# Kernel tuning notes

Measured on AMD Instinct MI355X. Metric: run time of the kernel, lower is better.

## Reference

```python
import jax, jax.numpy as jnp
import numpy as np

N, DIN, DH, W = 256, 256, 512, 8

def _conv(x, w):
    # x: [N,C,H,W], w: [O,I,3,3], VALID conv (input already reflection-padded)
    return jax.lax.conv_general_dilated(x, w, (1, 1), 'VALID',
                                        dimension_numbers=('NCHW', 'OIHW', 'NCHW'))

def setup_inputs() -> dict:
    key = jax.random.key(0)
    ks = jax.random.split(key, 16)
    def cw(k, o, i):
        return jax.random.normal(k, (o, i, 3, 3), jnp.float32) * 0.02
    def cb(k, o):
        return jax.random.normal(k, (o,), jnp.float32) * 0.02
    return {
        'input': jax.random.normal(ks[0], (N, DIN, W, W), jnp.float32),
        'hidden_state': jax.random.normal(ks[1], (N, 2, DH, W, W), jnp.float32),
        'w_ii': cw(ks[2], DH, DIN), 'w_if': cw(ks[3], DH, DIN),
        'w_ig': cw(ks[4], DH, DIN), 'w_io': cw(ks[5], DH, DIN),
        'w_hi': cw(ks[6], DH, DH), 'w_hf': cw(ks[7], DH, DH),
        'w_hg': cw(ks[8], DH, DH), 'w_ho': cw(ks[9], DH, DH),
        'b_i': cb(ks[10], DH), 'b_f': cb(ks[11], DH),
        'b_g': cb(ks[12], DH), 'b_o': cb(ks[13], DH),
        'Wc_i': jax.random.normal(ks[14], (1, DH, W, W), jnp.float32) * 0.02,
        'Wc_f': jax.random.normal(ks[15], (1, DH, W, W), jnp.float32) * 0.02,
        'Wc_o': jax.random.normal(jax.random.fold_in(key, 99), (1, DH, W, W), jnp.float32) * 0.02,
    }

def reference(input, hidden_state, w_ii, w_if, w_ig, w_io, w_hi, w_hf, w_hg, w_ho,
              b_i, b_f, b_g, b_o, Wc_i, Wc_f, Wc_o):
    h0 = hidden_state[:, 0]
    c0 = hidden_state[:, 1]
    pad = ((0, 0), (0, 0), (1, 1), (1, 1))
    xp = jnp.pad(input, pad, mode='reflect')
    hp = jnp.pad(h0, pad, mode='reflect')
    # Fuse the 4 input convs and 4 hidden convs into two conv calls (linearity => same math).
    w_x = jnp.concatenate([w_ii, w_if, w_ig, w_io], axis=0)   # [4*DH, DIN, 3, 3]
    w_h = jnp.concatenate([w_hi, w_hf, w_hg, w_ho], axis=0)   # [4*DH, DH, 3, 3]
    b = jnp.concatenate([b_i, b_f, b_g, b_o], axis=0)         # [4*DH]
    pre = _conv(xp, w_x) + _conv(hp, w_h) + b[None, :, None, None]  # [N, 4*DH, 8, 8]
    pi, pf, pg, po = jnp.split(pre, 4, axis=1)
    i = jax.nn.sigmoid(pi + c0 * Wc_i)
    f = jax.nn.sigmoid(pf + c0 * Wc_f)
    g = jnp.tanh(pg)
    c_t = f * c0 + i * g
    o = jax.nn.sigmoid(po + c_t * Wc_o)
    h_t = o * jnp.tanh(c_t)
    hidden_state_out = jnp.stack([h_t, c_t], axis=1)  # [N, 2, DH, 8, 8]
    return (o, hidden_state_out)
```

## Files before the change

kernel.cpp:

```cpp
#include <hip/hip_runtime.h>
#include <hip/hip_bf16.h>


#define DEVINL __device__ __forceinline__

typedef __attribute__((ext_vector_type(8))) short short8;
typedef __attribute__((ext_vector_type(4))) float f32x4;
typedef __attribute__((ext_vector_type(4))) float float4v;

DEVINL unsigned short f2bf(float f) {
  union { float f; unsigned u; } x; x.f = f;
  unsigned r = x.u + 0x7fffu + ((x.u >> 16) & 1u);
  return (unsigned short)(r >> 16);
}

DEVINL void async16(const void* g, void* l) {
  __builtin_amdgcn_global_load_lds((const __attribute__((address_space(1))) void*)g,
                                   (__attribute__((address_space(3))) void*)l,
                                   16, 0, 0);
}

__global__ void __launch_bounds__(256) pack_p(const float* __restrict__ input,
                                              const float* __restrict__ hs,
                                              unsigned short* __restrict__ P) {
  int idx = blockIdx.x * 256 + threadIdx.x;
  int c = idx % 768;
  int n = idx / 768;
  const float* src;
  if (c < 256) src = input + (size_t)(n * 256 + c) * 64;
  else         src = hs + (size_t)n * 65536 + (size_t)(c - 256) * 64;

  float v[64];
#pragma unroll
  for (int i = 0; i < 16; ++i) {
    float4v q = *(const float4v*)(src + i * 4);
    v[i * 4 + 0] = q.x; v[i * 4 + 1] = q.y; v[i * 4 + 2] = q.z; v[i * 4 + 3] = q.w;
  }
  unsigned short bv[64];
#pragma unroll
  for (int i = 0; i < 64; ++i) bv[i] = f2bf(v[i]);

  size_t base = (size_t)n * 76800 + c;
#pragma unroll
  for (int yp = 0; yp < 10; ++yp) {
    const int ys = (yp == 0) ? 1 : ((yp == 9) ? 6 : yp - 1);
#pragma unroll
    for (int xp = 0; xp < 10; ++xp) {
      const int xs = (xp == 0) ? 1 : ((xp == 9) ? 6 : xp - 1);
      P[base + (yp * 10 + xp) * 768] = bv[ys * 8 + xs];
    }
  }
}

__global__ void __launch_bounds__(256) pack_w(const float* __restrict__ wx0, const float* __restrict__ wx1,
                                              const float* __restrict__ wx2, const float* __restrict__ wx3,
                                              const float* __restrict__ wh0, const float* __restrict__ wh1,
                                              const float* __restrict__ wh2, const float* __restrict__ wh3,
                                              unsigned short* __restrict__ Wb) {
  int idx = blockIdx.x * 256 + threadIdx.x;
  int c = idx % 768;
  int co = idx / 768;
  int gate = co >> 9, och = co & 511;
  const float* w;
  size_t wbase;
  if (c < 256) {
    w = (gate == 0) ? wx0 : (gate == 1) ? wx1 : (gate == 2) ? wx2 : wx3;
    wbase = (size_t)(och * 256 + c) * 9;
  } else {
    w = (gate == 0) ? wh0 : (gate == 1) ? wh1 : (gate == 2) ? wh2 : wh3;
    wbase = (size_t)(och * 512 + (c - 256)) * 9;
  }
  float v[9];
#pragma unroll
  for (int s = 0; s < 9; ++s) v[s] = w[wbase + s];
  size_t ob = (size_t)co * 6912 + c;
#pragma unroll
  for (int ky = 0; ky < 3; ++ky)
#pragma unroll
    for (int kx = 0; kx < 3; ++kx)
      Wb[ob + ky * 2304 + kx * 768] = f2bf(v[ky * 3 + kx]);
}

#define NT 108

__global__ void __launch_bounds__(512, 2) gemm_pre(const unsigned short* __restrict__ P,
                                                   const unsigned short* __restrict__ W,
                                                   float* __restrict__ pre) {
  __shared__ __align__(16) unsigned short lds[65536];

  const int t = threadIdx.x;
  const int l = t & 63;
  const int wid = t >> 6;
  const int wr = wid >> 2, wc = wid & 3;
  const int lm = l & 15, lk = l >> 4;

  int bid = blockIdx.x;
  const int x8 = bid & 7, j = bid >> 3;
  const int mb = x8 * 8 + (j & 7);
  const int nb = j >> 3;

  const int strow = t >> 2;
  const int stk = (((t & 3) ^ ((t >> 3) & 3)) << 3);
  const int am0 = mb * 256 + strow;
  const int am1 = am0 + 128;
  const int awin0 = ((am0 >> 6) * 100 + ((am0 >> 3) & 7) * 10 + (am0 & 7)) * 768 + stk;
  const int awin1 = ((am1 >> 6) * 100 + ((am1 >> 3) & 7) * 10 + (am1 & 7)) * 768 + stk;
  const size_t bb0 = (size_t)(nb * 256 + strow) * 6912 + stk;
  const size_t bb1 = bb0 + (size_t)128 * 6912;
  const int dstT = t * 8;

  const int swz = ((lk ^ ((lm >> 1) & 3)) << 3);
  const int aoffb = (wr * 128 + lm) * 32 + swz;
  const int boffb = 32768 + (wc * 64 + lm) * 32 + swz;

#define STAGE_A(TS, KS, D) { \
    int kg = (TS) * 64 + (KS) * 32; \
    int ky = kg / 2304; \
    int off = kg + ky * 5376; \
    async16(P + awin0 + off, &lds[(D) * 16384 + (KS) * 8192 + dstT]); \
    async16(P + awin1 + off, &lds[(D) * 16384 + (KS) * 8192 + 4096 + dstT]); }

#define STAGE_B(TS, KS, D) { \
    int kg = (TS) * 64 + (KS) * 32; \
    async16(W + bb0 + kg, &lds[32768 + (D) * 16384 + (KS) * 8192 + dstT]); \
    async16(W + bb1 + kg, &lds[32768 + (D) * 16384 + (KS) * 8192 + 4096 + dstT]); }

#define DS_A(D, KS, M) (*(const short8*)&lds[(D) * 16384 + (KS) * 8192 + (M) * 512 + aoffb])
#define DS_B(D, KS, Nn) (*(const short8*)&lds[(D) * 16384 + (KS) * 8192 + (Nn) * 512 + boffb])

#define LGKM0 asm volatile("s_waitcnt lgkmcnt(0)" ::: "memory")
#define VMC8  asm volatile("s_waitcnt vmcnt(8)" ::: "memory")

  f32x4 acc[8][4];
#pragma unroll
  for (int i = 0; i < 8; ++i)
#pragma unroll
    for (int n2 = 0; n2 < 4; ++n2) acc[i][n2] = (f32x4){0.f, 0.f, 0.f, 0.f};

  short8 a[4], b[4];

  STAGE_A(0, 0, 0); STAGE_B(0, 0, 0);
  STAGE_A(0, 1, 0); STAGE_B(0, 1, 0);
  STAGE_A(1, 0, 1); STAGE_B(1, 0, 1);
  VMC8;
  __builtin_amdgcn_s_barrier();

#define MFMA_BLK(MB) \
  _Pragma("unroll") for (int mm = 0; mm < 4; ++mm) \
  _Pragma("unroll") for (int nn = 0; nn < 4; ++nn) \
    acc[(MB) + mm][nn] = __builtin_amdgcn_mfma_f32_16x16x32_bf16(a[mm], b[nn], acc[(MB) + mm][nn], 0, 0, 0);

#pragma unroll 2
  for (int tau = 0; tau < NT; ++tau) {
    const int d = tau & 1;
    int t1 = tau + 1; if (t1 >= NT) t1 -= NT;
    int t2 = tau + 2; if (t2 >= NT) t2 -= NT;

#pragma unroll
    for (int mm = 0; mm < 4; ++mm) a[mm] = DS_A(d, 0, mm);
#pragma unroll
    for (int nn = 0; nn < 4; ++nn) b[nn] = DS_B(d, 0, nn);
    STAGE_A(t1, 1, d ^ 1);
    __builtin_amdgcn_s_barrier();
    LGKM0;
    __builtin_amdgcn_s_setprio(1);
    MFMA_BLK(0);
    __builtin_amdgcn_s_setprio(0);
    __builtin_amdgcn_s_barrier();

#pragma unroll
    for (int mm = 0; mm < 4; ++mm) a[mm] = DS_A(d, 0, 4 + mm);
    STAGE_B(t1, 1, d ^ 1);
    __builtin_amdgcn_s_barrier();
    LGKM0;
    __builtin_amdgcn_s_setprio(1);
    MFMA_BLK(4);
    __builtin_amdgcn_s_setprio(0);
    VMC8;
    __builtin_amdgcn_s_barrier();

#pragma unroll
    for (int mm = 0; mm < 4; ++mm) a[mm] = DS_A(d, 1, mm);
#pragma unroll
    for (int nn = 0; nn < 4; ++nn) b[nn] = DS_B(d, 1, nn);
    STAGE_A(t2, 0, d);
    __builtin_amdgcn_s_barrier();
    LGKM0;
    __builtin_amdgcn_s_setprio(1);
    MFMA_BLK(0);
    __builtin_amdgcn_s_setprio(0);
    __builtin_amdgcn_s_barrier();

#pragma unroll
    for (int mm = 0; mm < 4; ++mm) a[mm] = DS_A(d, 1, 4 + mm);
    STAGE_B(t2, 0, d);
    __builtin_amdgcn_s_barrier();
    LGKM0;
    __builtin_amdgcn_s_setprio(1);
    MFMA_BLK(4);
    __builtin_amdgcn_s_setprio(0);
    VMC8;
    __builtin_amdgcn_s_barrier();
  }

  const int r0 = mb * 256 + wr * 128 + lk * 4;
  const int cb = nb * 256 + wc * 64 + lm;
#pragma unroll
  for (int mm = 0; mm < 8; ++mm)
#pragma unroll
    for (int nn = 0; nn < 4; ++nn)
#pragma unroll
      for (int r = 0; r < 4; ++r)
        pre[(size_t)(r0 + mm * 16 + r) * 2048 + cb + nn * 16] = acc[mm][nn][r];
}

__global__ void __launch_bounds__(256) lstm_pointwise(const float* __restrict__ pre,
                                                      const float* __restrict__ hs,
                                                      const float* __restrict__ bi, const float* __restrict__ bf_,
                                                      const float* __restrict__ bg, const float* __restrict__ bo,
                                                      const float* __restrict__ wci, const float* __restrict__ wcf,
                                                      const float* __restrict__ wco,
                                                      float* __restrict__ out) {
  __shared__ float g[4][64][65];
  const int blk = blockIdx.x;
  const int n = blk >> 3, chb = blk & 7;
  const int t = threadIdx.x;

  {
    const int chl = t & 63, pr = t >> 6;
#pragma unroll
    for (int it = 0; it < 16; ++it) {
      int p = it * 4 + pr;
      size_t rowb = (size_t)(n * 64 + p) * 2048 + chb * 64 + chl;
      g[0][p][chl] = pre[rowb];
      g[1][p][chl] = pre[rowb + 512];
      g[2][p][chl] = pre[rowb + 1024];
      g[3][p][chl] = pre[rowb + 1536];
    }
  }
  __syncthreads();
  {
    const int pl = t & 63, chr = t >> 6;
#pragma unroll 4
    for (int it = 0; it < 16; ++it) {
      int chi = it * 4 + chr;
      int ch = chb * 64 + chi;
      int sp = ch * 64 + pl;
      float c0 = hs[(size_t)n * 65536 + 32768 + sp];
      float pi = g[0][pl][chi] + bi[ch];
      float pf = g[1][pl][chi] + bf_[ch];
      float pg = g[2][pl][chi] + bg[ch];
      float po = g[3][pl][chi] + bo[ch];
      float ig = 1.f / (1.f + __expf(-(pi + c0 * wci[sp])));
      float fg = 1.f / (1.f + __expf(-(pf + c0 * wcf[sp])));
      float gg = tanhf(pg);
      float ct = fg * c0 + ig * gg;
      float og = 1.f / (1.f + __expf(-(po + ct * wco[sp])));
      float ht = og * tanhf(ct);
      out[(size_t)(n * 512 + ch) * 64 + pl] = og;
      float* hso = out + 8388608;
      hso[(size_t)(n * 1024 + ch) * 64 + pl] = ht;
      hso[(size_t)(n * 1024 + 512 + ch) * 64 + pl] = ct;
    }
  }
}

extern "C" void kernel_launch(void* const* d_in, const int* in_sizes, int n_in,
                              void* d_out, int out_size, void* d_ws, size_t ws_size,
                              hipStream_t stream) {
  const float* input = (const float*)d_in[0];
  const float* hs    = (const float*)d_in[1];
  const float* wx0 = (const float*)d_in[2];
  const float* wx1 = (const float*)d_in[3];
  const float* wx2 = (const float*)d_in[4];
  const float* wx3 = (const float*)d_in[5];
  const float* wh0 = (const float*)d_in[6];
  const float* wh1 = (const float*)d_in[7];
  const float* wh2 = (const float*)d_in[8];
  const float* wh3 = (const float*)d_in[9];
  const float* bi  = (const float*)d_in[10];
  const float* bf_ = (const float*)d_in[11];
  const float* bg  = (const float*)d_in[12];
  const float* bo  = (const float*)d_in[13];
  const float* wci = (const float*)d_in[14];
  const float* wcf = (const float*)d_in[15];
  const float* wco = (const float*)d_in[16];
  float* out = (float*)d_out;

  float*          pre = (float*)d_ws;
  unsigned short* P   = (unsigned short*)((char*)d_ws + 134217728u);
  unsigned short* Wb  = (unsigned short*)((char*)d_ws + 134217728u + 39321600u);

  pack_p<<<768, 256, 0, stream>>>(input, hs, P);
  pack_w<<<6144, 256, 0, stream>>>(wx0, wx1, wx2, wx3, wh0, wh1, wh2, wh3, Wb);
  gemm_pre<<<512, 512, 0, stream>>>(P, Wb, pre);
  lstm_pointwise<<<2048, 256, 0, stream>>>(pre, hs, bi, bf_, bg, bo, wci, wcf, wco, out);
}
```

Baseline: 655.5 us.

## Fuse LSTM pointwise epilogue into GEMM by interleaving gate columns in weights

Reorders packed weight rows so that each 64-column group holds the i,f,g,o gates of 16 channels, which puts all four gates for one channel in the same wave's accumulators. The pointwise LSTM math then runs directly in the GEMM epilogue. This removes the 128MB fp32 pre-activation round trip and the separate pointwise kernel launch. It also swaps tanhf for an exp-based tanh, and the epilogue stores and c0/peephole loads are less coalesced than before.

```diff
diff --git a/kernel.cpp b/kernel.cpp
--- a/kernel.cpp
+++ b/kernel.cpp
@@ -13,6 +13,9 @@
   unsigned r = x.u + 0x7fffu + ((x.u >> 16) & 1u);
   return (unsigned short)(r >> 16);
 }
+
+DEVINL float sigm(float x) { return 1.f / (1.f + __expf(-x)); }
+DEVINL float tanh_fast(float x) { return 1.f - 2.f / (1.f + __expf(2.f * x)); }
 
 DEVINL void async16(const void* g, void* l) {
   __builtin_amdgcn_global_load_lds((const __attribute__((address_space(1))) void*)g,
@@ -73,7 +76,8 @@
   float v[9];
 #pragma unroll
   for (int s = 0; s < 9; ++s) v[s] = w[wbase + s];
-  size_t ob = (size_t)co * 6912 + c;
+  const int crow = (och >> 4) * 64 + gate * 16 + (och & 15);
+  size_t ob = (size_t)crow * 6912 + c;
 #pragma unroll
   for (int ky = 0; ky < 3; ++ky)
 #pragma unroll
@@ -83,9 +87,14 @@
 
 #define NT 108
 
-__global__ void __launch_bounds__(512, 2) gemm_pre(const unsigned short* __restrict__ P,
-                                                   const unsigned short* __restrict__ W,
-                                                   float* __restrict__ pre) {
+__global__ void __launch_bounds__(512, 2) gemm_lstm(const unsigned short* __restrict__ P,
+                                                    const unsigned short* __restrict__ W,
+                                                    const float* __restrict__ hs,
+                                                    const float* __restrict__ b_i, const float* __restrict__ b_f,
+                                                    const float* __restrict__ b_g, const float* __restrict__ b_o,
+                                                    const float* __restrict__ wci, const float* __restrict__ wcf,
+                                                    const float* __restrict__ wco,
+                                                    float* __restrict__ out) {
   __shared__ __align__(16) unsigned short lds[65536];
 
   const int t = threadIdx.x;
@@ -203,64 +212,31 @@
     __builtin_amdgcn_s_barrier();
   }
 
-  const int r0 = mb * 256 + wr * 128 + lk * 4;
-  const int cb = nb * 256 + wc * 64 + lm;
-#pragma unroll
-  for (int mm = 0; mm < 8; ++mm)
-#pragma unroll
-    for (int nn = 0; nn < 4; ++nn)
-#pragma unroll
-      for (int r = 0; r < 4; ++r)
-        pre[(size_t)(r0 + mm * 16 + r) * 2048 + cb + nn * 16] = acc[mm][nn][r];
-}
-
-__global__ void __launch_bounds__(256) lstm_pointwise(const float* __restrict__ pre,
-                                                      const float* __restrict__ hs,
-                                                      const float* __restrict__ bi, const float* __restrict__ bf_,
-                                                      const float* __restrict__ bg, const float* __restrict__ bo,
-                                                      const float* __restrict__ wci, const float* __restrict__ wcf,
-                                                      const float* __restrict__ wco,
-                                                      float* __restrict__ out) {
-  __shared__ float g[4][64][65];
-  const int blk = blockIdx.x;
-  const int n = blk >> 3, chb = blk & 7;
-  const int t = threadIdx.x;
-
-  {
-    const int chl = t & 63, pr = t >> 6;
-#pragma unroll
-    for (int it = 0; it < 16; ++it) {
-      int p = it * 4 + pr;
-      size_t rowb = (size_t)(n * 64 + p) * 2048 + chb * 64 + chl;
-      g[0][p][chl] = pre[rowb];
-      g[1][p][chl] = pre[rowb + 512];
-      g[2][p][chl] = pre[rowb + 1024];
-      g[3][p][chl] = pre[rowb + 1536];
-    }
-  }
-  __syncthreads();
-  {
-    const int pl = t & 63, chr = t >> 6;
-#pragma unroll 4
-    for (int it = 0; it < 16; ++it) {
-      int chi = it * 4 + chr;
-      int ch = chb * 64 + chi;
-      int sp = ch * 64 + pl;
-      float c0 = hs[(size_t)n * 65536 + 32768 + sp];
-      float pi = g[0][pl][chi] + bi[ch];
-      float pf = g[1][pl][chi] + bf_[ch];
-      float pg = g[2][pl][chi] + bg[ch];
-      float po = g[3][pl][chi] + bo[ch];
-      float ig = 1.f / (1.f + __expf(-(pi + c0 * wci[sp])));
-      float fg = 1.f / (1.f + __expf(-(pf + c0 * wcf[sp])));
-      float gg = tanhf(pg);
-      float ct = fg * c0 + ig * gg;
-      float og = 1.f / (1.f + __expf(-(po + ct * wco[sp])));
-      float ht = og * tanhf(ct);
-      out[(size_t)(n * 512 + ch) * 64 + pl] = og;
-      float* hso = out + 8388608;
-      hso[(size_t)(n * 1024 + ch) * 64 + pl] = ht;
-      hso[(size_t)(n * 1024 + 512 + ch) * 64 + pl] = ct;
+  const int ch = (nb * 4 + wc) * 16 + lm;
+  const int chp = ch * 64;
+  const float bI = b_i[ch], bF = b_f[ch], bG = b_g[ch], bO = b_o[ch];
+  float* hso = out + 8388608;
+#pragma unroll
+  for (int mm = 0; mm < 8; ++mm) {
+    const int n = mb * 4 + wr * 2 + (mm >> 2);
+    const float* c0p = hs + (size_t)n * 65536 + 32768 + chp;
+#pragma unroll
+    for (int r = 0; r < 4; ++r) {
+      const int p = (mm & 3) * 16 + lk * 4 + r;
+      const float c0 = c0p[p];
+      const float pi = acc[mm][0][r] + bI;
+      const float pf = acc[mm][1][r] + bF;
+      const float pg = acc[mm][2][r] + bG;
+      const float po = acc[mm][3][r] + bO;
+      const float ig = sigm(pi + c0 * wci[chp + p]);
+      const float fg = sigm(pf + c0 * wcf[chp + p]);
+      const float gg = tanh_fast(pg);
+      const float ct = fg * c0 + ig * gg;
+      const float og = sigm(po + ct * wco[chp + p]);
+      const float ht = og * tanh_fast(ct);
+      out[(size_t)n * 32768 + chp + p] = og;
+      hso[(size_t)n * 65536 + chp + p] = ht;
+      hso[(size_t)n * 65536 + 32768 + chp + p] = ct;
     }
   }
 }
@@ -287,12 +263,10 @@
   const float* wco = (const float*)d_in[16];
   float* out = (float*)d_out;
 
-  float*          pre = (float*)d_ws;
-  unsigned short* P   = (unsigned short*)((char*)d_ws + 134217728u);
-  unsigned short* Wb  = (unsigned short*)((char*)d_ws + 134217728u + 39321600u);
+  unsigned short* P  = (unsigned short*)d_ws;
+  unsigned short* Wb = (unsigned short*)((char*)d_ws + 39321600u);
 
   pack_p<<<768, 256, 0, stream>>>(input, hs, P);
   pack_w<<<6144, 256, 0, stream>>>(wx0, wx1, wx2, wx3, wh0, wh1, wh2, wh3, Wb);
-  gemm_pre<<<512, 512, 0, stream>>>(P, Wb, pre);
-  lstm_pointwise<<<2048, 256, 0, stream>>>(pre, hs, bi, bf_, bg, bo, wci, wcf, wco, out);
-}
+  gemm_lstm<<<512, 512, 0, stream>>>(P, Wb, hs, bi, bf_, bg, bo, wci, wcf, wco, out);
+}
```

Result: faster. 641.0 us (-2.2%).
